# Kernel tuning notes

Measured on AMD Instinct MI355X. Metric: run time of the kernel, lower is better.

## Reference

```python
import jax, jax.numpy as jnp
import numpy as np

D_CONV = 4  # matches Mamba(d_conv=4)


def _silu(v):
    return v * jax.nn.sigmoid(v)


def _mamba_block(x, in_w, cw, cb, xw, dtw, dtb, A_log, Dp, ow):
    # x: (B, L, d_model)
    B, L, _ = x.shape
    d_inner, d_state = A_log.shape
    xz = x @ in_w.T                        # (B, L, 2*d_inner)
    xr, z = jnp.split(xz, 2, axis=-1)      # each (B, L, d_inner)
    # causal depthwise conv1d (pad d_conv-1 on the left, truncate to L)
    xp = jnp.pad(xr, ((0, 0), (D_CONV - 1, 0), (0, 0)))
    xc = sum(xp[:, k:k + L, :] * cw[:, k] for k in range(D_CONV)) + cb
    xc = _silu(xc)                         # (B, L, d_inner)
    dbl = xc @ xw.T                        # (B, L, dt_rank + 2*d_state)
    dt_rank = dbl.shape[-1] - 2 * d_state
    dt, Bm, Cm = jnp.split(dbl, [dt_rank, dt_rank + d_state], axis=-1)
    dt = jax.nn.softplus(dt @ dtw.T + dtb)  # (B, L, d_inner)
    A = -jnp.exp(A_log)                    # (d_inner, d_state)
    dA = jnp.exp(dt[..., None] * A)                          # (B, L, d_inner, d_state)
    dBx = dt[..., None] * Bm[:, :, None, :] * xc[..., None]  # (B, L, d_inner, d_state)

    def step(h, inputs):
        dA_t, dBx_t, C_t = inputs          # (B,d,s), (B,d,s), (B,s)
        h = dA_t * h + dBx_t
        y = jnp.einsum('bds,bs->bd', h, C_t)
        return h, y

    h0 = jnp.zeros((B, d_inner, d_state), x.dtype)
    _, ys = jax.lax.scan(step, h0, (dA.transpose(1, 0, 2, 3),
                                    dBx.transpose(1, 0, 2, 3),
                                    Cm.transpose(1, 0, 2)))
    y = ys.transpose(1, 0, 2) + xc * Dp    # skip term D*u
    y = y * _silu(z)                       # gated
    return y @ ow.T                        # (B, L, d_model)


def setup_inputs() -> dict:
    key = jax.random.key(0)
    d_model, d_state, n_layer = 1024, 16, 2
    d_inner = 2 * d_model
    dt_rank = d_model // 16  # ceil(1024/16)
    Bsz, L = 2, 1024
    ks = jax.random.split(key, 8)
    s = 0.02
    x = jax.random.normal(ks[0], (Bsz, L, d_model), jnp.float32)
    in_proj_w = jax.random.normal(ks[1], (n_layer, 2 * d_inner, d_model), jnp.float32) * s
    conv_w = jax.random.normal(ks[2], (n_layer, d_inner, D_CONV), jnp.float32) * 0.2
    conv_b = jnp.zeros((n_layer, d_inner), jnp.float32)
    x_proj_w = jax.random.normal(ks[3], (n_layer, dt_rank + 2 * d_state, d_inner), jnp.float32) * s
    dt_proj_w = jax.random.normal(ks[4], (n_layer, d_inner, dt_rank), jnp.float32) * s
    dt_proj_b = jax.random.uniform(ks[5], (n_layer, d_inner), jnp.float32, -5.0, -3.0)
    A_log = jnp.log(jnp.tile(jnp.arange(1, d_state + 1, dtype=jnp.float32), (n_layer, d_inner, 1)))
    D = jnp.ones((n_layer, d_inner), jnp.float32)
    out_proj_w = jax.random.normal(ks[6], (n_layer, d_model, d_inner), jnp.float32) * s
    return {"x": x, "in_proj_w": in_proj_w, "conv_w": conv_w, "conv_b": conv_b,
            "x_proj_w": x_proj_w, "dt_proj_w": dt_proj_w, "dt_proj_b": dt_proj_b,
            "A_log": A_log, "D": D, "out_proj_w": out_proj_w}


def reference(x, in_proj_w, conv_w, conv_b, x_proj_w, dt_proj_w, dt_proj_b, A_log, D, out_proj_w):
    n_layer = in_proj_w.shape[0]
    for i in range(n_layer):
        x = _mamba_block(x, in_proj_w[i], conv_w[i], conv_b[i], x_proj_w[i],
                         dt_proj_w[i], dt_proj_b[i], A_log[i], D[i], out_proj_w[i])
    return x
```

## Files before the change

kernel.cpp:

```cpp
#include <hip/hip_runtime.h>
#include <hip/hip_bf16.h>
#include <cmath>

typedef __bf16 bf16x8_t __attribute__((ext_vector_type(8)));
typedef float  f32x4_t  __attribute__((ext_vector_type(4)));
using bf16 = __hip_bfloat16;

#define LOG2E 1.44269504088896340736f
#define LN2   0.69314718055994530942f

#define AS1C(p) ((const __attribute__((address_space(1))) void*)(p))
#define AS3C(p) ((__attribute__((address_space(3))) void*)(p))

__device__ __forceinline__ float fexp2(float x) { return __builtin_amdgcn_exp2f(x); }
__device__ __forceinline__ float flog2(float x) { return __builtin_amdgcn_logf(x); }
__device__ __forceinline__ float frcp (float x) { return __builtin_amdgcn_rcpf(x); }

__global__ __launch_bounds__(256)
void cast_multi(const float* s0, bf16* d0, int e0,
                const float* s1, bf16* d1, int e1,
                const float* s2, bf16* d2, int e2,
                const float* s3, bf16* d3, int e3,
                const float* s4, bf16* d4, int e4)
{
    const int blk = blockIdx.x;
    const float* src; bf16* dst; int base;
    if      (blk < e0) { src = s0; dst = d0; base = blk; }
    else if (blk < e1) { src = s1; dst = d1; base = blk - e0; }
    else if (blk < e2) { src = s2; dst = d2; base = blk - e1; }
    else if (blk < e3) { src = s3; dst = d3; base = blk - e2; }
    else               { src = s4; dst = d4; base = blk - e3; }

    const int i = base * 256 + threadIdx.x;
    const float4* s = (const float4*)(src + (size_t)i * 8);
    float4 a = s[0], b = s[1];
    bf16 o[8];
    o[0] = __float2bfloat16(a.x); o[1] = __float2bfloat16(a.y);
    o[2] = __float2bfloat16(a.z); o[3] = __float2bfloat16(a.w);
    o[4] = __float2bfloat16(b.x); o[5] = __float2bfloat16(b.y);
    o[6] = __float2bfloat16(b.z); o[7] = __float2bfloat16(b.w);
    *(int4*)(dst + (size_t)i * 8) = *(int4*)o;
}

template<int MODE, bool SPLITK>
__global__ __launch_bounds__(256)
void gemm_bf16(const bf16* __restrict__ A, const bf16* __restrict__ B,
               float* __restrict__ Cf, bf16* __restrict__ Cb,
               int M, int N, int K, int lda, int ldb, int ldc)
{
    __shared__ __align__(16) bf16 At[2][64][32];
    __shared__ __align__(16) bf16 Bt[2][128][32];

    const int tid  = threadIdx.x;
    const int lane = tid & 63;
    const int wid  = tid >> 6;
    const int wr2  = wid & 1;
    const int wc2  = wid >> 1;
    const int fr   = lane & 15;
    const int fq   = lane >> 4;

    const int row0 = blockIdx.y * 64;
    const int col0 = blockIdx.x * 128;
    const int kb   = SPLITK ? blockIdx.z * K : 0;

    const int gA_row = wid * 16 + (lane >> 2);
    const int gB_row = wid * 32 + (lane >> 2);
    const int g_kp   = (((lane & 3) ^ ((lane >> 3) & 3)) * 8);
    const bf16* aP0 = A + (size_t)(row0 + gA_row) * lda + g_kp + kb;
    int bR0 = col0 + gB_row;      if (bR0 >= N) bR0 = N - 1;
    int bR1 = col0 + gB_row + 16; if (bR1 >= N) bR1 = N - 1;
    const bf16* bP0 = B + (size_t)bR0 * ldb + g_kp + kb;
    const bf16* bP1 = B + (size_t)bR1 * ldb + g_kp + kb;

    const int rchunk = (fq ^ ((fr >> 1) & 3)) * 8;

    f32x4_t acc[2][4];
    #pragma unroll
    for (int m = 0; m < 2; ++m)
        #pragma unroll
        for (int n = 0; n < 4; ++n)
            acc[m][n] = f32x4_t{0.f, 0.f, 0.f, 0.f};

    auto STAGE = [&](int buf, int k0) {
        __builtin_amdgcn_global_load_lds(AS1C(aP0 + k0), AS3C(&At[buf][wid * 16][0]),      16, 0, 0);
        __builtin_amdgcn_global_load_lds(AS1C(bP0 + k0), AS3C(&Bt[buf][wid * 32][0]),      16, 0, 0);
        __builtin_amdgcn_global_load_lds(AS1C(bP1 + k0), AS3C(&Bt[buf][wid * 32 + 16][0]), 16, 0, 0);
    };

    STAGE(0, 0);
    __syncthreads();
    int cur = 0;
    for (int k0 = 0; k0 < K; k0 += 32) {
        if (k0 + 32 < K) STAGE(cur ^ 1, k0 + 32);

        bf16x8_t af[2], bg[4];
        #pragma unroll
        for (int m = 0; m < 2; ++m)
            af[m] = *(const bf16x8_t*)&At[cur][wr2 * 32 + m * 16 + fr][rchunk];
        #pragma unroll
        for (int n = 0; n < 4; ++n)
            bg[n] = *(const bf16x8_t*)&Bt[cur][wc2 * 64 + n * 16 + fr][rchunk];
        #pragma unroll
        for (int m = 0; m < 2; ++m)
            #pragma unroll
            for (int n = 0; n < 4; ++n)
                acc[m][n] = __builtin_amdgcn_mfma_f32_16x16x32_bf16(
                    af[m], bg[n], acc[m][n], 0, 0, 0);

        __syncthreads();
        cur ^= 1;
    }

    float* Cfz = SPLITK ? (Cf + (size_t)blockIdx.z * M * ldc) : Cf;

    #pragma unroll
    for (int m = 0; m < 2; ++m) {
        #pragma unroll
        for (int n = 0; n < 4; ++n) {
            const int c = col0 + wc2 * 64 + n * 16 + fr;
            if (c < N) {
                #pragma unroll
                for (int r = 0; r < 4; ++r) {
                    const int rr = row0 + wr2 * 32 + m * 16 + fq * 4 + r;
                    if (SPLITK || MODE != 1) Cfz[(size_t)rr * ldc + c] = acc[m][n][r];
                    if (!SPLITK && MODE != 0) Cb[(size_t)rr * ldc + c] = __float2bfloat16(acc[m][n][r]);
                }
            }
        }
    }
}

__global__ __launch_bounds__(256)
void reduce_pk(const float* __restrict__ part, float* __restrict__ of,
               bf16* __restrict__ oh, int n4, int stride4, int S)
{
    const int i = blockIdx.x * blockDim.x + threadIdx.x;
    if (i >= n4) return;
    const float4* p4 = (const float4*)part;
    float4 s = p4[i];
    for (int k = 1; k < S; ++k) {
        float4 v = p4[(size_t)k * stride4 + i];
        s.x += v.x; s.y += v.y; s.z += v.z; s.w += v.w;
    }
    if (of) ((float4*)of)[i] = s;
    if (oh) {
        bf16 o[4];
        o[0] = __float2bfloat16(s.x); o[1] = __float2bfloat16(s.y);
        o[2] = __float2bfloat16(s.z); o[3] = __float2bfloat16(s.w);
        *(int2*)(oh + (size_t)i * 4) = *(int2*)o;
    }
}

__global__ __launch_bounds__(256)
void conv_silu(const bf16* __restrict__ xz, const float* __restrict__ cw,
               const float* __restrict__ cb, bf16* __restrict__ xc,
               int Bsz, int L, int dinner)
{
    const int nv = dinner / 4;
    const int L4 = L / 4;
    const int g  = blockIdx.x * blockDim.x + threadIdx.x;
    const int d4 = (g % nv) * 4;
    const int t4 = (g / nv) % L4;
    const int b  = g / (nv * L4);
    if (b >= Bsz) return;

    const int t0 = t4 * 4;
    const int ldxz = 2 * dinner;

    float4 w0 = *(const float4*)(cw + (size_t)(d4 + 0) * 4);
    float4 w1 = *(const float4*)(cw + (size_t)(d4 + 1) * 4);
    float4 w2 = *(const float4*)(cw + (size_t)(d4 + 2) * 4);
    float4 w3 = *(const float4*)(cw + (size_t)(d4 + 3) * 4);
    float4 bias = *(const float4*)(cb + d4);

    float4 r[7];
    const bf16* base = xz + (size_t)b * L * ldxz + d4;
    #pragma unroll
    for (int k = 0; k < 7; ++k) {
        const int ts = t0 - 3 + k;
        if (ts >= 0 && ts < L) {
            const bf16* rp = base + (size_t)ts * ldxz;
            r[k] = make_float4(__bfloat162float(rp[0]), __bfloat162float(rp[1]),
                               __bfloat162float(rp[2]), __bfloat162float(rp[3]));
        } else {
            r[k] = make_float4(0.f, 0.f, 0.f, 0.f);
        }
    }

    bf16* outp = xc + ((size_t)b * L + t0) * dinner + d4;
    #pragma unroll
    for (int j = 0; j < 4; ++j) {
        float4 acc = bias;
        #pragma unroll
        for (int k = 0; k < 4; ++k) {
            const float4 v = r[j + k];
            acc.x = fmaf(v.x, (&w0.x)[k], acc.x);
            acc.y = fmaf(v.y, (&w1.x)[k], acc.y);
            acc.z = fmaf(v.z, (&w2.x)[k], acc.z);
            acc.w = fmaf(v.w, (&w3.x)[k], acc.w);
        }
        acc.x = acc.x * frcp(1.f + fexp2(-acc.x * LOG2E));
        acc.y = acc.y * frcp(1.f + fexp2(-acc.y * LOG2E));
        acc.z = acc.z * frcp(1.f + fexp2(-acc.z * LOG2E));
        acc.w = acc.w * frcp(1.f + fexp2(-acc.w * LOG2E));
        bf16 o[4];
        o[0] = __float2bfloat16(acc.x); o[1] = __float2bfloat16(acc.y);
        o[2] = __float2bfloat16(acc.z); o[3] = __float2bfloat16(acc.w);
        *(int2*)(outp + (size_t)j * dinner) = *(int2*)o;
    }
}

__global__ __launch_bounds__(256)
void scan_part1(const bf16* __restrict__ dtraw, const bf16* __restrict__ xc,
                const float* __restrict__ dbl, const float* __restrict__ dtb,
                const float* __restrict__ alog, float* __restrict__ hend,
                float* __restrict__ Ssum, int Bsz, int L, int dinner,
                int NC, int CL)
{
    const int g = blockIdx.x * blockDim.x + threadIdx.x;
    const int d = g % dinner;
    const int c = (g / dinner) % NC;
    const int b = g / (dinner * NC);
    if (b >= Bsz) return;

    const float* ap = alog + (size_t)d * 16;
    float a_[16];
    *(float4*)&a_[0]  = *(const float4*)(ap + 0);
    *(float4*)&a_[4]  = *(const float4*)(ap + 4);
    *(float4*)&a_[8]  = *(const float4*)(ap + 8);
    *(float4*)&a_[12] = *(const float4*)(ap + 12);
    float As[16];
    #pragma unroll
    for (int i = 0; i < 16; ++i) As[i] = -fexp2(a_[i] * LOG2E) * LOG2E;
    const float bias = dtb[d];

    const int t0 = c * CL;
    const bf16*  dt_p = dtraw + ((size_t)b * L + t0) * dinner + d;
    const bf16*  xc_p = xc    + ((size_t)b * L + t0) * dinner + d;
    const float* bl_p = dbl   + ((size_t)b * L + t0) * 96 + 64;

    float h[16];
    #pragma unroll
    for (int i = 0; i < 16; ++i) h[i] = 0.f;
    float S = 0.f;

    for (int t = 0; t < CL; ++t) {
        const float dtv = __bfloat162float(*dt_p);
        const float xcv = __bfloat162float(*xc_p);
        float Bv[16];
        *(float4*)&Bv[0]  = *(const float4*)(bl_p + 0);
        *(float4*)&Bv[4]  = *(const float4*)(bl_p + 4);
        *(float4*)&Bv[8]  = *(const float4*)(bl_p + 8);
        *(float4*)&Bv[12] = *(const float4*)(bl_p + 12);

        const float xv = dtv + bias;
        const float e  = fexp2(xv * LOG2E);
        const float sp = (xv > 15.f) ? xv : LN2 * flog2(1.f + e);
        S += sp;
        const float u = sp * xcv;
        #pragma unroll
        for (int i = 0; i < 16; ++i)
            h[i] = fmaf(fexp2(sp * As[i]), h[i], u * Bv[i]);

        dt_p += dinner; xc_p += dinner; bl_p += 96;
    }

    const size_t idx = ((size_t)b * NC + c) * dinner + d;
    float* hp = hend + idx * 16;
    *(float4*)(hp + 0)  = make_float4(h[0],  h[1],  h[2],  h[3]);
    *(float4*)(hp + 4)  = make_float4(h[4],  h[5],  h[6],  h[7]);
    *(float4*)(hp + 8)  = make_float4(h[8],  h[9],  h[10], h[11]);
    *(float4*)(hp + 12) = make_float4(h[12], h[13], h[14], h[15]);
    Ssum[idx] = S;
}

__global__ __launch_bounds__(256)
void chunk_prefix(float* __restrict__ hend, const float* __restrict__ Ssum,
                  const float* __restrict__ alog, int Bsz, int dinner, int NC)
{
    const int g = blockIdx.x * blockDim.x + threadIdx.x;
    const int s = g & 15;
    const int d = (g >> 4) % dinner;
    const int b = g / (16 * dinner);
    if (b >= Bsz) return;

    const float As2 = -fexp2(alog[(size_t)d * 16 + s] * LOG2E) * LOG2E;

    size_t idx = (size_t)b * NC * dinner + d;
    float he = hend[idx * 16 + s];
    float Sv = Ssum[idx];
    float h = 0.f;
    for (int c = 0; c < NC; ++c) {
        float heN = 0.f, SvN = 0.f;
        if (c + 1 < NC) {
            heN = hend[(idx + dinner) * 16 + s];
            SvN = Ssum[idx + dinner];
        }
        hend[idx * 16 + s] = h;
        h = fmaf(fexp2(As2 * Sv), h, he);
        he = heN; Sv = SvN; idx += dinner;
    }
}

__global__ __launch_bounds__(256)
void scan_part2(bf16* dty, const bf16* __restrict__ xc,
                const float* __restrict__ dbl, const bf16* __restrict__ xz,
                const float* __restrict__ dtb, const float* __restrict__ alog,
                const float* __restrict__ Dp, const float* __restrict__ hinit,
                int Bsz, int L, int dinner, int NC, int CL)
{
    const int g = blockIdx.x * blockDim.x + threadIdx.x;
    const int d = g % dinner;
    const int c = (g / dinner) % NC;
    const int b = g / (dinner * NC);
    if (b >= Bsz) return;

    const float* ap = alog + (size_t)d * 16;
    float a_[16];
    *(float4*)&a_[0]  = *(const float4*)(ap + 0);
    *(float4*)&a_[4]  = *(const float4*)(ap + 4);
    *(float4*)&a_[8]  = *(const float4*)(ap + 8);
    *(float4*)&a_[12] = *(const float4*)(ap + 12);
    float As[16];
    #pragma unroll
    for (int i = 0; i < 16; ++i) As[i] = -fexp2(a_[i] * LOG2E) * LOG2E;
    const float bias = dtb[d];
    const float Dval = Dp[d];

    const size_t cidx = ((size_t)b * NC + c) * dinner + d;
    float h[16];
    const float* hp = hinit + cidx * 16;
    *(float4*)&h[0]  = *(const float4*)(hp + 0);
    *(float4*)&h[4]  = *(const float4*)(hp + 4);
    *(float4*)&h[8]  = *(const float4*)(hp + 8);
    *(float4*)&h[12] = *(const float4*)(hp + 12);

    const int t0 = c * CL;
    bf16*        dt_p = dty + ((size_t)b * L + t0) * dinner + d;
    const bf16*  xc_p = xc  + ((size_t)b * L + t0) * dinner + d;
    const float* bl_p = dbl + ((size_t)b * L + t0) * 96 + 64;
    const bf16*  z_p  = xz  + ((size_t)b * L + t0) * (2 * dinner) + dinner + d;

    for (int t = 0; t < CL; ++t) {
        const float dtv = __bfloat162float(*dt_p);
        const float xcv = __bfloat162float(*xc_p);
        const float zv  = __bfloat162float(*z_p);
        float Bv[16], Cv[16];
        *(float4*)&Bv[0]  = *(const float4*)(bl_p + 0);
        *(float4*)&Bv[4]  = *(const float4*)(bl_p + 4);
        *(float4*)&Bv[8]  = *(const float4*)(bl_p + 8);
        *(float4*)&Bv[12] = *(const float4*)(bl_p + 12);
        *(float4*)&Cv[0]  = *(const float4*)(bl_p + 16);
        *(float4*)&Cv[4]  = *(const float4*)(bl_p + 20);
        *(float4*)&Cv[8]  = *(const float4*)(bl_p + 24);
        *(float4*)&Cv[12] = *(const float4*)(bl_p + 28);

        const float xv = dtv + bias;
        const float e  = fexp2(xv * LOG2E);
        const float sp = (xv > 15.f) ? xv : LN2 * flog2(1.f + e);
        const float u = sp * xcv;
        float y = 0.f;
        #pragma unroll
        for (int i = 0; i < 16; ++i) {
            h[i] = fmaf(fexp2(sp * As[i]), h[i], u * Bv[i]);
            y = fmaf(h[i], Cv[i], y);
        }

        y = fmaf(xcv, Dval, y);
        const float sig = frcp(1.f + fexp2(-zv * LOG2E));
        *dt_p = __float2bfloat16(y * (zv * sig));

        dt_p += dinner; xc_p += dinner; bl_p += 96; z_p += 2 * dinner;
    }
}

extern "C" void kernel_launch(void* const* d_in, const int* in_sizes, int n_in,
                              void* d_out, int out_size, void* d_ws, size_t ws_size,
                              hipStream_t stream)
{
    const float* x    = (const float*)d_in[0];
    const float* inw  = (const float*)d_in[1];
    const float* cw   = (const float*)d_in[2];
    const float* cb   = (const float*)d_in[3];
    const float* xw   = (const float*)d_in[4];
    const float* dtw  = (const float*)d_in[5];
    const float* dtb  = (const float*)d_in[6];
    const float* alog = (const float*)d_in[7];
    const float* Dp   = (const float*)d_in[8];
    const float* ow   = (const float*)d_in[9];
    float* out = (float*)d_out;

    const int Bsz = 2, L = 1024, dmodel = 1024, dinner = 2048;
    const int BL = Bsz * L;
    const int NC = 32, CL = L / NC;
    const int SPX = 16, KSX = dinner / SPX;
    const int SPO = 2,  KSO = dinner / SPO;

    char* p = (char*)d_ws;
    auto alloc = [&](size_t bytes) { char* r = p; p += (bytes + 63) & ~size_t(63); return r; };
    bf16*  wb_in  = (bf16*) alloc((size_t)2 * 2 * dinner * dmodel * 2);
    bf16*  wb_x   = (bf16*) alloc((size_t)2 * 96 * dinner * 2);
    bf16*  wb_dt  = (bf16*) alloc((size_t)2 * dinner * 64 * 2);
    bf16*  wb_ow  = (bf16*) alloc((size_t)2 * dmodel * dinner * 2);
    bf16*  curb   = (bf16*) alloc((size_t)BL * dmodel * 2);
    bf16*  xzb16  = (bf16*) alloc((size_t)BL * 2 * dinner * 2);
    bf16*  xcb16  = (bf16*) alloc((size_t)BL * dinner * 2);
    float* dblb   = (float*)alloc((size_t)BL * 96 * 4);
    bf16*  dblb16 = (bf16*) alloc((size_t)BL * 96 * 2);
    bf16*  dtrb16 = (bf16*) alloc((size_t)BL * dinner * 2);
    float* ssumb  = (float*)alloc((size_t)Bsz * NC * dinner * 4);
    float* partb  = (float*)alloc((size_t)SPO * BL * dmodel * 4);
    float* hendb  = partb;

    const int scan_blocks = (Bsz * NC * dinner) / 256;
    const int pfx_blocks  = (Bsz * dinner * 16) / 256;

    {
        const int n8_x  = BL * dmodel / 8;
        const int n8_in = 2 * 2 * dinner * dmodel / 8;
        const int n8_xw = 2 * 96 * dinner / 8;
        const int n8_dt = 2 * dinner * 64 / 8;
        const int n8_ow = 2 * dmodel * dinner / 8;
        const int e0 = n8_x / 256;
        const int e1 = e0 + n8_in / 256;
        const int e2 = e1 + n8_xw / 256;
        const int e3 = e2 + n8_dt / 256;
        const int e4 = e3 + n8_ow / 256;
        cast_multi<<<e4, 256, 0, stream>>>(
            x, curb, e0, inw, wb_in, e1, xw, wb_x, e2, dtw, wb_dt, e3, ow, wb_ow, e4);
    }

    for (int l = 0; l < 2; ++l) {
        const bf16*  wb_in_l = wb_in + (size_t)l * 2 * dinner * dmodel;
        const bf16*  wb_x_l  = wb_x  + (size_t)l * 96 * dinner;
        const bf16*  wb_dt_l = wb_dt + (size_t)l * dinner * 64;
        const bf16*  wb_ow_l = wb_ow + (size_t)l * dmodel * dinner;
        const float* cw_l    = cw   + (size_t)l * dinner * 4;
        const float* cb_l    = cb   + (size_t)l * dinner;
        const float* dtb_l   = dtb  + (size_t)l * dinner;
        const float* alog_l  = alog + (size_t)l * dinner * 16;
        const float* Dp_l    = Dp   + (size_t)l * dinner;

        gemm_bf16<1, false><<<dim3(2 * dinner / 128, BL / 64), 256, 0, stream>>>(
            curb, wb_in_l, nullptr, xzb16, BL, 2 * dinner, dmodel, dmodel, dmodel, 2 * dinner);

        conv_silu<<<(Bsz * (L / 4) * (dinner / 4)) / 256, 256, 0, stream>>>(
            xzb16, cw_l, cb_l, xcb16, Bsz, L, dinner);

        gemm_bf16<0, true><<<dim3(1, BL / 64, SPX), 256, 0, stream>>>(
            xcb16, wb_x_l, partb, nullptr, BL, 96, KSX, dinner, dinner, 96);
        reduce_pk<<<(BL * 96 / 4 + 255) / 256, 256, 0, stream>>>(
            partb, dblb, dblb16, BL * 96 / 4, BL * 96 / 4, SPX);

        gemm_bf16<1, false><<<dim3(dinner / 128, BL / 64), 256, 0, stream>>>(
            dblb16, wb_dt_l, nullptr, dtrb16, BL, dinner, 64, 96, 64, dinner);

        scan_part1<<<scan_blocks, 256, 0, stream>>>(
            dtrb16, xcb16, dblb, dtb_l, alog_l, hendb, ssumb, Bsz, L, dinner, NC, CL);
        chunk_prefix<<<pfx_blocks, 256, 0, stream>>>(
            hendb, ssumb, alog_l, Bsz, dinner, NC);
        scan_part2<<<scan_blocks, 256, 0, stream>>>(
            dtrb16, xcb16, dblb, xzb16, dtb_l, alog_l, Dp_l, hendb,
            Bsz, L, dinner, NC, CL);

        gemm_bf16<0, true><<<dim3(dmodel / 128, BL / 64, SPO), 256, 0, stream>>>(
            dtrb16, wb_ow_l, partb, nullptr, BL, dmodel, KSO, dinner, dinner, dmodel);
        if (l == 0)
            reduce_pk<<<(BL * dmodel / 4 + 255) / 256, 256, 0, stream>>>(
                partb, nullptr, curb, BL * dmodel / 4, BL * dmodel / 4, SPO);
        else
            reduce_pk<<<(BL * dmodel / 4 + 255) / 256, 256, 0, stream>>>(
                partb, out, nullptr, BL * dmodel / 4, BL * dmodel / 4, SPO);
    }
}
```

Baseline: 319.9 us.

## Split scan state across thread pairs and double chunk count

Each scan thread now handles 8 of the 16 state dimensions, with a pair of lanes covering one channel, and partial outputs are combined with a lane shuffle. The number of chunks is raised from 32 to 64, so each chunk is shorter. Together these give four times as many threads, which should improve occupancy and latency hiding in the sequential scan kernels. In exchange, the per-step dt/xc/z loads and softplus are done twice per channel, the prefix kernel has more chunks to walk serially, and the chunk-state buffer grows.

```diff
diff --git a/kernel.cpp b/kernel.cpp
--- a/kernel.cpp
+++ b/kernel.cpp
@@ -217,41 +217,38 @@
                 float* __restrict__ Ssum, int Bsz, int L, int dinner,
                 int NC, int CL)
 {
-    const int g = blockIdx.x * blockDim.x + threadIdx.x;
-    const int d = g % dinner;
-    const int c = (g / dinner) % NC;
-    const int b = g / (dinner * NC);
+    const int g  = blockIdx.x * blockDim.x + threadIdx.x;
+    const int s8 = g & 1;
+    const int d  = (g >> 1) % dinner;
+    const int c  = ((g >> 1) / dinner) % NC;
+    const int b  = g / (2 * dinner * NC);
     if (b >= Bsz) return;
 
-    const float* ap = alog + (size_t)d * 16;
-    float a_[16];
-    *(float4*)&a_[0]  = *(const float4*)(ap + 0);
-    *(float4*)&a_[4]  = *(const float4*)(ap + 4);
-    *(float4*)&a_[8]  = *(const float4*)(ap + 8);
-    *(float4*)&a_[12] = *(const float4*)(ap + 12);
-    float As[16];
-    #pragma unroll
-    for (int i = 0; i < 16; ++i) As[i] = -fexp2(a_[i] * LOG2E) * LOG2E;
+    const float* ap = alog + (size_t)d * 16 + s8 * 8;
+    float a_[8];
+    *(float4*)&a_[0] = *(const float4*)(ap + 0);
+    *(float4*)&a_[4] = *(const float4*)(ap + 4);
+    float As[8];
+    #pragma unroll
+    for (int i = 0; i < 8; ++i) As[i] = -fexp2(a_[i] * LOG2E) * LOG2E;
     const float bias = dtb[d];
 
     const int t0 = c * CL;
     const bf16*  dt_p = dtraw + ((size_t)b * L + t0) * dinner + d;
     const bf16*  xc_p = xc    + ((size_t)b * L + t0) * dinner + d;
-    const float* bl_p = dbl   + ((size_t)b * L + t0) * 96 + 64;
-
-    float h[16];
-    #pragma unroll
-    for (int i = 0; i < 16; ++i) h[i] = 0.f;
+    const float* bl_p = dbl   + ((size_t)b * L + t0) * 96 + 64 + s8 * 8;
+
+    float h[8];
+    #pragma unroll
+    for (int i = 0; i < 8; ++i) h[i] = 0.f;
     float S = 0.f;
 
     for (int t = 0; t < CL; ++t) {
         const float dtv = __bfloat162float(*dt_p);
         const float xcv = __bfloat162float(*xc_p);
-        float Bv[16];
-        *(float4*)&Bv[0]  = *(const float4*)(bl_p + 0);
-        *(float4*)&Bv[4]  = *(const float4*)(bl_p + 4);
-        *(float4*)&Bv[8]  = *(const float4*)(bl_p + 8);
-        *(float4*)&Bv[12] = *(const float4*)(bl_p + 12);
+        float Bv[8];
+        *(float4*)&Bv[0] = *(const float4*)(bl_p + 0);
+        *(float4*)&Bv[4] = *(const float4*)(bl_p + 4);
 
         const float xv = dtv + bias;
         const float e  = fexp2(xv * LOG2E);
@@ -259,19 +256,17 @@
         S += sp;
         const float u = sp * xcv;
         #pragma unroll
-        for (int i = 0; i < 16; ++i)
+        for (int i = 0; i < 8; ++i)
             h[i] = fmaf(fexp2(sp * As[i]), h[i], u * Bv[i]);
 
         dt_p += dinner; xc_p += dinner; bl_p += 96;
     }
 
     const size_t idx = ((size_t)b * NC + c) * dinner + d;
-    float* hp = hend + idx * 16;
-    *(float4*)(hp + 0)  = make_float4(h[0],  h[1],  h[2],  h[3]);
-    *(float4*)(hp + 4)  = make_float4(h[4],  h[5],  h[6],  h[7]);
-    *(float4*)(hp + 8)  = make_float4(h[8],  h[9],  h[10], h[11]);
-    *(float4*)(hp + 12) = make_float4(h[12], h[13], h[14], h[15]);
-    Ssum[idx] = S;
+    float* hp = hend + idx * 16 + s8 * 8;
+    *(float4*)(hp + 0) = make_float4(h[0], h[1], h[2], h[3]);
+    *(float4*)(hp + 4) = make_float4(h[4], h[5], h[6], h[7]);
+    if (s8 == 0) Ssum[idx] = S;
 }
 
 __global__ __launch_bounds__(256)
@@ -309,51 +304,44 @@
                 const float* __restrict__ Dp, const float* __restrict__ hinit,
                 int Bsz, int L, int dinner, int NC, int CL)
 {
-    const int g = blockIdx.x * blockDim.x + threadIdx.x;
-    const int d = g % dinner;
-    const int c = (g / dinner) % NC;
-    const int b = g / (dinner * NC);
+    const int g  = blockIdx.x * blockDim.x + threadIdx.x;
+    const int s8 = g & 1;
+    const int d  = (g >> 1) % dinner;
+    const int c  = ((g >> 1) / dinner) % NC;
+    const int b  = g / (2 * dinner * NC);
     if (b >= Bsz) return;
 
-    const float* ap = alog + (size_t)d * 16;
-    float a_[16];
-    *(float4*)&a_[0]  = *(const float4*)(ap + 0);
-    *(float4*)&a_[4]  = *(const float4*)(ap + 4);
-    *(float4*)&a_[8]  = *(const float4*)(ap + 8);
-    *(float4*)&a_[12] = *(const float4*)(ap + 12);
-    float As[16];
-    #pragma unroll
-    for (int i = 0; i < 16; ++i) As[i] = -fexp2(a_[i] * LOG2E) * LOG2E;
+    const float* ap = alog + (size_t)d * 16 + s8 * 8;
+    float a_[8];
+    *(float4*)&a_[0] = *(const float4*)(ap + 0);
+    *(float4*)&a_[4] = *(const float4*)(ap + 4);
+    float As[8];
+    #pragma unroll
+    for (int i = 0; i < 8; ++i) As[i] = -fexp2(a_[i] * LOG2E) * LOG2E;
     const float bias = dtb[d];
     const float Dval = Dp[d];
 
     const size_t cidx = ((size_t)b * NC + c) * dinner + d;
-    float h[16];
-    const float* hp = hinit + cidx * 16;
-    *(float4*)&h[0]  = *(const float4*)(hp + 0);
-    *(float4*)&h[4]  = *(const float4*)(hp + 4);
-    *(float4*)&h[8]  = *(const float4*)(hp + 8);
-    *(float4*)&h[12] = *(const float4*)(hp + 12);
+    float h[8];
+    const float* hp = hinit + cidx * 16 + s8 * 8;
+    *(float4*)&h[0] = *(const float4*)(hp + 0);
+    *(float4*)&h[4] = *(const float4*)(hp + 4);
 
     const int t0 = c * CL;
     bf16*        dt_p = dty + ((size_t)b * L + t0) * dinner + d;
     const bf16*  xc_p = xc  + ((size_t)b * L + t0) * dinner + d;
-    const float* bl_p = dbl + ((size_t)b * L + t0) * 96 + 64;
+    const float* bl_p = dbl + ((size_t)b * L + t0) * 96 + 64 + s8 * 8;
     const bf16*  z_p  = xz  + ((size_t)b * L + t0) * (2 * dinner) + dinner + d;
 
     for (int t = 0; t < CL; ++t) {
         const float dtv = __bfloat162float(*dt_p);
         const float xcv = __bfloat162float(*xc_p);
         const float zv  = __bfloat162float(*z_p);
-        float Bv[16], Cv[16];
-        *(float4*)&Bv[0]  = *(const float4*)(bl_p + 0);
-        *(float4*)&Bv[4]  = *(const float4*)(bl_p + 4);
-        *(float4*)&Bv[8]  = *(const float4*)(bl_p + 8);
-        *(float4*)&Bv[12] = *(const float4*)(bl_p + 12);
-        *(float4*)&Cv[0]  = *(const float4*)(bl_p + 16);
-        *(float4*)&Cv[4]  = *(const float4*)(bl_p + 20);
-        *(float4*)&Cv[8]  = *(const float4*)(bl_p + 24);
-        *(float4*)&Cv[12] = *(const float4*)(bl_p + 28);
+        float Bv[8], Cv[8];
+        *(float4*)&Bv[0] = *(const float4*)(bl_p + 0);
+        *(float4*)&Bv[4] = *(const float4*)(bl_p + 4);
+        *(float4*)&Cv[0] = *(const float4*)(bl_p + 16);
+        *(float4*)&Cv[4] = *(const float4*)(bl_p + 20);
 
         const float xv = dtv + bias;
         const float e  = fexp2(xv * LOG2E);
@@ -361,14 +349,17 @@
         const float u = sp * xcv;
         float y = 0.f;
         #pragma unroll
-        for (int i = 0; i < 16; ++i) {
+        for (int i = 0; i < 8; ++i) {
             h[i] = fmaf(fexp2(sp * As[i]), h[i], u * Bv[i]);
             y = fmaf(h[i], Cv[i], y);
         }
-
-        y = fmaf(xcv, Dval, y);
-        const float sig = frcp(1.f + fexp2(-zv * LOG2E));
-        *dt_p = __float2bfloat16(y * (zv * sig));
+        y += __shfl_xor(y, 1);
+
+        if (s8 == 0) {
+            y = fmaf(xcv, Dval, y);
+            const float sig = frcp(1.f + fexp2(-zv * LOG2E));
+            *dt_p = __float2bfloat16(y * (zv * sig));
+        }
 
         dt_p += dinner; xc_p += dinner; bl_p += 96; z_p += 2 * dinner;
     }
@@ -392,7 +383,7 @@
 
     const int Bsz = 2, L = 1024, dmodel = 1024, dinner = 2048;
     const int BL = Bsz * L;
-    const int NC = 32, CL = L / NC;
+    const int NC = 64, CL = L / NC;
     const int SPX = 16, KSX = dinner / SPX;
     const int SPO = 2,  KSO = dinner / SPO;
 
@@ -412,7 +403,7 @@
     float* partb  = (float*)alloc((size_t)SPO * BL * dmodel * 4);
     float* hendb  = partb;
 
-    const int scan_blocks = (Bsz * NC * dinner) / 256;
+    const int scan_blocks = (Bsz * NC * dinner * 2) / 256;
     const int pfx_blocks  = (Bsz * dinner * 16) / 256;
 
     {
```

New measurement: 303.3 us. 1.05x faster.
